# Optimization experiments

Measured on AMD Instinct MI355X. Metric: run time of the kernel, lower is better.

The kernel has to match this reference:

```python
import jax, jax.numpy as jnp
import numpy as np
import math

E, H, KH, F = 2048, 32, 8, 8192
HD = E // H          # 64
KV = KH * HD         # 512
B, S = 2, 2048
EPS = 1e-5


def _rope_table(seq_len, head_dim, base=10000.0):
    inv = 1.0 / (base ** (np.arange(0, head_dim, 2, dtype=np.float32) / head_dim))
    t = np.arange(seq_len, dtype=np.float32)
    fr = np.outer(t, inv)                               # [S, HD/2]
    return jnp.asarray(np.stack([np.cos(fr), np.sin(fr)], axis=-1))  # [S, HD/2, 2]


def setup_inputs() -> dict:
    key = jax.random.key(0)
    ks = jax.random.split(key, 8)
    x = jax.random.normal(ks[0], (B, S, E), dtype=jnp.float32)
    attention_mask = jnp.tril(jnp.ones((1, 1, S, S), dtype=bool))  # causal
    freqs_cis = _rope_table(S, HD)                                  # [S, 32, 2]
    sc = 0.02
    w_qkv = jax.random.normal(ks[1], (E + 2 * KV, E), dtype=jnp.float32) * sc
    w_o = jax.random.normal(ks[2], (E, E), dtype=jnp.float32) * sc
    w1 = jax.random.normal(ks[3], (F, E), dtype=jnp.float32) * sc
    w3 = jax.random.normal(ks[4], (F, E), dtype=jnp.float32) * sc
    w2 = jax.random.normal(ks[5], (E, F), dtype=jnp.float32) * sc
    attn_norm_w = jnp.ones((E,), dtype=jnp.float32)
    ff_norm_w = jnp.ones((E,), dtype=jnp.float32)
    return {"x": x, "attention_mask": attention_mask, "freqs_cis": freqs_cis,
            "w_qkv": w_qkv, "w_o": w_o, "w1": w1, "w2": w2, "w3": w3,
            "attn_norm_w": attn_norm_w, "ff_norm_w": ff_norm_w}


def _rmsnorm(x, w):
    xf = x.astype(jnp.float32)
    n = xf * jax.lax.rsqrt(jnp.mean(xf * xf, axis=-1, keepdims=True) + EPS)
    return n.astype(x.dtype) * w


def _apply_rope(x, freqs_cis):
    # x: [B, h, S, HD]; freqs_cis: [S, HD/2, 2] broadcasting over B, h
    xf = x.astype(jnp.float32).reshape(*x.shape[:-1], -1, 2)
    c, s = freqs_cis[..., 0], freqs_cis[..., 1]
    x0, x1 = xf[..., 0], xf[..., 1]
    out = jnp.stack([x0 * c - x1 * s, x1 * c + x0 * s], axis=-1)
    return out.reshape(x.shape).astype(x.dtype)


def reference(x, attention_mask, freqs_cis, w_qkv, w_o, w1, w2, w3, attn_norm_w, ff_norm_w):
    bs, seq = x.shape[:2]
    h = _rmsnorm(x, attn_norm_w)
    qkv = h @ w_qkv.T                                   # [B, S, E + 2*KV]
    q, k, v = jnp.split(qkv, [E, E + KV], axis=-1)
    q = q.reshape(bs, seq, H, HD).transpose(0, 2, 1, 3)   # [B, H, S, HD]
    k = k.reshape(bs, seq, KH, HD).transpose(0, 2, 1, 3)  # [B, KH, S, HD]
    v = v.reshape(bs, seq, KH, HD).transpose(0, 2, 1, 3)
    q = _apply_rope(q, freqs_cis)
    k = _apply_rope(k, freqs_cis)
    rep = H // KH
    k = jnp.repeat(k, rep, axis=1)                        # [B, H, S, HD]
    v = jnp.repeat(v, rep, axis=1)
    score = jnp.einsum('bhqd,bhkd->bhqk', q, k) / math.sqrt(HD)
    score = jnp.where(attention_mask, score, -jnp.inf)
    attn = jax.nn.softmax(score, axis=-1)
    o = jnp.einsum('bhqk,bhkd->bhqd', attn, v)
    o = o.transpose(0, 2, 1, 3).reshape(bs, seq, E) @ w_o.T
    h2 = x + o
    g = _rmsnorm(h2, ff_norm_w)
    ff = (jax.nn.silu(g @ w1.T) * (g @ w3.T)) @ w2.T
    return h2 + ff
```

## Files before the change

kernel.cpp:

```cpp
#include <hip/hip_runtime.h>
#include <hip/hip_bf16.h>
#include <cstdint>
#include <cstddef>

typedef __bf16 bf16;
typedef __bf16 bf16x2 __attribute__((ext_vector_type(2)));
typedef __bf16 bf16x4 __attribute__((ext_vector_type(4)));
typedef __bf16 bf16x8 __attribute__((ext_vector_type(8)));
typedef float f32x4 __attribute__((ext_vector_type(4)));
typedef float f32x16 __attribute__((ext_vector_type(16)));

#define EDIM 2048
#define SEQ  2048
#define BATCH 2
#define NH   32
#define NKV  8
#define HD   64
#define FF   8192
#define NTOK 4096
#define QKVN 3072

__device__ __forceinline__ void gld_lds16(const void* gp, void* lp) {
    __builtin_amdgcn_global_load_lds(
        (__attribute__((address_space(1))) void*)(gp),
        (__attribute__((address_space(3))) void*)(lp), 16, 0, 0);
}

__global__ __launch_bounds__(256)
void cvt_f32_bf16(const float* __restrict__ in, bf16* __restrict__ out, long n4) {
    long i = (long)blockIdx.x * blockDim.x + threadIdx.x;
    long stride = (long)gridDim.x * blockDim.x;
    for (; i < n4; i += stride) {
        float4 v = ((const float4*)in)[i];
        bf16x4 o;
        o[0] = (bf16)v.x; o[1] = (bf16)v.y; o[2] = (bf16)v.z; o[3] = (bf16)v.w;
        ((bf16x4*)out)[i] = o;
    }
}

__global__ __launch_bounds__(256)
void rmsnorm_bf16(const float* __restrict__ x, const float* __restrict__ w,
                  bf16* __restrict__ out) {
    __shared__ float red[4];
    const int row = blockIdx.x;
    const long base = (long)row * EDIM;
    const int t = threadIdx.x;
    float4 v0 = *(const float4*)(x + base + t * 4);
    float4 v1 = *(const float4*)(x + base + 1024 + t * 4);
    float ss = v0.x*v0.x + v0.y*v0.y + v0.z*v0.z + v0.w*v0.w
             + v1.x*v1.x + v1.y*v1.y + v1.z*v1.z + v1.w*v1.w;
    #pragma unroll
    for (int off = 1; off < 64; off <<= 1) ss += __shfl_xor(ss, off, 64);
    if ((t & 63) == 0) red[t >> 6] = ss;
    __syncthreads();
    float tot = red[0] + red[1] + red[2] + red[3];
    float inv = rsqrtf(tot * (1.0f / EDIM) + 1e-5f);
    float4 w0 = *(const float4*)(w + t * 4);
    float4 w1 = *(const float4*)(w + 1024 + t * 4);
    bf16x4 o0, o1;
    o0[0] = (bf16)(v0.x * inv * w0.x); o0[1] = (bf16)(v0.y * inv * w0.y);
    o0[2] = (bf16)(v0.z * inv * w0.z); o0[3] = (bf16)(v0.w * inv * w0.w);
    o1[0] = (bf16)(v1.x * inv * w1.x); o1[1] = (bf16)(v1.y * inv * w1.y);
    o1[2] = (bf16)(v1.z * inv * w1.z); o1[3] = (bf16)(v1.w * inv * w1.w);
    *(bf16x4*)(out + base + t * 4) = o0;
    *(bf16x4*)(out + base + 1024 + t * 4) = o1;
}

template<int EPI>
__global__ __launch_bounds__(256, 2)
void gemm_nt(const bf16* __restrict__ A, const bf16* __restrict__ B,
             void* __restrict__ Cv, const float* __restrict__ res,
             int M, int N, int K) {
    __shared__ bf16 As[128 * 32];
    __shared__ bf16 Bs[128 * 32];
    const int tid = threadIdx.x;
    const int lane = tid & 63;
    const int wave = tid >> 6;
    const int wm = (wave >> 1) * 64;
    const int wn = (wave & 1) * 64;

    int gx = gridDim.x, gy = gridDim.y;
    int bx = blockIdx.x, by = blockIdx.y;
    int nwg = gx * gy;
    if (((nwg & 63) | (gx & 7) | (gy & 7)) == 0) {
        int l = bx + gx * by;
        int nl = (l & 7) * (nwg >> 3) + (l >> 3);
        int s = nl >> 6, r = nl & 63;
        int spr = gx >> 3;
        bx = (s % spr) * 8 + (r & 7);
        by = (s / spr) * 8 + (r >> 3);
    }
    const int bm = by * 128;
    const int bn = bx * 128;
    const int lrow = lane & 15;
    const int koff = (lane >> 4) * 8;

    f32x4 acc[4][4] = {};

    for (int k0 = 0; k0 < K; k0 += 32) {
        __syncthreads();
        #pragma unroll
        for (int t = 0; t < 2; ++t) {
            int c = tid + t * 256;
            int r = c >> 2;
            int kc = (c & 3) * 8;
            gld_lds16(A + (long)(bm + r) * K + k0 + kc, As + c * 8);
            gld_lds16(B + (long)(bn + r) * K + k0 + kc, Bs + c * 8);
        }
        __syncthreads();
        bf16x8 af[4], bfr[4];
        #pragma unroll
        for (int t = 0; t < 4; ++t) {
            af[t]  = *(const bf16x8*)(As + (wm + t * 16 + lrow) * 32 + koff);
            bfr[t] = *(const bf16x8*)(Bs + (wn + t * 16 + lrow) * 32 + koff);
        }
        #pragma unroll
        for (int i = 0; i < 4; ++i)
            #pragma unroll
            for (int j = 0; j < 4; ++j)
                acc[i][j] = __builtin_amdgcn_mfma_f32_16x16x32_bf16(af[i], bfr[j], acc[i][j], 0, 0, 0);
    }

    const int row0 = bm + wm + (lane >> 4) * 4;
    const int col0 = bn + wn + (lane & 15);
    #pragma unroll
    for (int i = 0; i < 4; ++i) {
        #pragma unroll
        for (int j = 0; j < 4; ++j) {
            int col = col0 + j * 16;
            #pragma unroll
            for (int r = 0; r < 4; ++r) {
                long idx = (long)(row0 + i * 16 + r) * N + col;
                float v = acc[i][j][r];
                if (EPI == 0) {
                    ((float*)Cv)[idx] = v;
                } else if (EPI == 1) {
                    ((bf16*)Cv)[idx] = (bf16)v;
                } else if (EPI == 2) {
                    ((float*)Cv)[idx] = v + res[idx];
                } else {
                    float u = (float)((bf16*)Cv)[idx];
                    float sl = u / (1.0f + __expf(-u));
                    ((bf16*)Cv)[idx] = (bf16)(sl * v);
                }
            }
        }
    }
}

__global__ __launch_bounds__(256)
void rope_prep(const bf16* __restrict__ qkv, const float* __restrict__ fr,
               bf16* __restrict__ Qo, bf16* __restrict__ Ko) {
    const int row = blockIdx.x;
    const int b = row >> 11, s = row & 2047;
    const int t = threadIdx.x;
    const long rbase = (long)row * QKVN;
    #pragma unroll
    for (int i = 0; i < 4; ++i) {
        int p = t + i * 256;
        int hh = p >> 5, d = p & 31;
        bf16x2 xv = *(const bf16x2*)(qkv + rbase + hh * 64 + 2 * d);
        float x0 = (float)xv[0], x1 = (float)xv[1];
        float2 cs = *(const float2*)(fr + (long)(s * 32 + d) * 2);
        bf16x2 o;
        o[0] = (bf16)((x0 * cs.x - x1 * cs.y) * 0.125f);
        o[1] = (bf16)((x1 * cs.x + x0 * cs.y) * 0.125f);
        *(bf16x2*)(Qo + ((long)(b * NH + hh) * SEQ + s) * HD + 2 * d) = o;
    }
    {
        int kh = t >> 5, d = t & 31;
        bf16x2 xv = *(const bf16x2*)(qkv + rbase + EDIM + kh * 64 + 2 * d);
        float x0 = (float)xv[0], x1 = (float)xv[1];
        float2 cs = *(const float2*)(fr + (long)(s * 32 + d) * 2);
        bf16x2 o;
        o[0] = (bf16)(x0 * cs.x - x1 * cs.y);
        o[1] = (bf16)(x1 * cs.x + x0 * cs.y);
        *(bf16x2*)(Ko + ((long)(b * NKV + kh) * SEQ + s) * HD + 2 * d) = o;
    }
}

__global__ __launch_bounds__(256)
void v_prep(const bf16* __restrict__ qkv, bf16* __restrict__ Vt) {
    __shared__ bf16 tile[64 * 72];
    const int blk = blockIdx.x;
    const int b = blk >> 8;
    const int kvh = (blk >> 5) & 7;
    const int st = blk & 31;
    const int t = threadIdx.x;
    #pragma unroll
    for (int i = 0; i < 2; ++i) {
        int c = t + i * 256;
        int kk = c >> 3, hdo = (c & 7) * 8;
        bf16x8 v = *(const bf16x8*)(qkv + (long)(b * SEQ + st * 64 + kk) * QKVN + 2560 + kvh * 64 + hdo);
        *(bf16x8*)(tile + kk * 72 + hdo) = v;
    }
    __syncthreads();
    const long obase = ((long)(b * NKV + kvh) * 32 + st) * 4096;
    #pragma unroll
    for (int i = 0; i < 2; ++i) {
        int c = t + i * 256;
        int hd = c >> 3, ko = (c & 7) * 8;
        bf16x8 v;
        #pragma unroll
        for (int j = 0; j < 8; ++j) v[j] = tile[(ko + j) * 72 + hd];
        *(bf16x8*)(Vt + obase + hd * 64 + ko) = v;
    }
}

__global__ __launch_bounds__(256, 3)
void attn_fwd(const bf16* __restrict__ Q, const bf16* __restrict__ K,
              const bf16* __restrict__ Vt, bf16* __restrict__ Out) {
    __shared__ bf16 Ps[4][32][40];
    const int tid = threadIdx.x, lane = tid & 63, w = tid >> 6;
    const int bh = blockIdx.x;
    const int qt = blockIdx.y;
    const int b = bh >> 5, h = bh & 31;
    const int kvh = h >> 2;
    const int ql = lane & 31;
    const int hh = lane >> 5;
    const int sw = (ql ^ (ql >> 3)) & 3;
    const int q0 = qt * 128 + w * 32;
    const int qmax = q0 + 31;
    const long qbase  = ((long)(b * NH + h) * SEQ + q0) * HD;
    const long kvbase = ((long)(b * NKV + kvh) * SEQ) * HD;
    bf16* Pw = &Ps[w][0][0];

    bf16x8 qa[4];
    #pragma unroll
    for (int ds = 0; ds < 4; ++ds)
        qa[ds] = *(const bf16x8*)(Q + qbase + (long)ql * HD + ds * 16 + hh * 8);

    f32x16 oacc[2] = {};
    float mi = -1e30f, li = 0.f;

    const int nt64 = qt * 2 + 1 + (w >> 1);
    for (int kt = 0; kt < nt64; ++kt) {
        const bf16* Kt  = K  + kvbase + (long)kt * (64 * HD);
        const bf16* Vtt = Vt + kvbase + (long)kt * 4096;
        bf16x8 ka[2][4], va[2][2][2];
        #pragma unroll
        for (int h2 = 0; h2 < 2; ++h2)
            #pragma unroll
            for (int ds = 0; ds < 4; ++ds)
                ka[h2][ds] = *(const bf16x8*)(Kt + (h2 * 32 + ql) * HD + ds * 16 + hh * 8);
        #pragma unroll
        for (int h2 = 0; h2 < 2; ++h2)
            #pragma unroll
            for (int t = 0; t < 2; ++t)
                #pragma unroll
                for (int c = 0; c < 2; ++c)
                    va[h2][t][c] = *(const bf16x8*)(Vtt + (t * 32 + ql) * 64 + h2 * 32 + c * 16 + hh * 8);
        const bool lastt = (kt == nt64 - 1);
        #pragma unroll
        for (int h2 = 0; h2 < 2; ++h2) {
            if (h2 == 1 && kt * 64 + 32 > qmax) break;
            f32x16 s = {};
            #pragma unroll
            for (int ds = 0; ds < 4; ++ds)
                s = __builtin_amdgcn_mfma_f32_32x32x16_bf16(ka[h2][ds], qa[ds], s, 0, 0, 0);
            if (lastt) {
                #pragma unroll
                for (int r = 0; r < 16; ++r) {
                    int kk = kt * 64 + h2 * 32 + (r & 3) + 8 * (r >> 2) + 4 * hh;
                    if (kk > q0 + ql) s[r] = -1e30f;
                }
            }
            float tmax = s[0];
            #pragma unroll
            for (int r = 1; r < 16; ++r) tmax = fmaxf(tmax, s[r]);
            tmax = fmaxf(tmax, __shfl_xor(tmax, 32, 64));
            if (!__all(tmax <= mi)) {
                float mnew = fmaxf(mi, tmax);
                float alpha = __expf(mi - mnew);
                li *= alpha;
                #pragma unroll
                for (int r = 0; r < 16; ++r) { oacc[0][r] *= alpha; oacc[1][r] *= alpha; }
                mi = mnew;
            }
            float psum = 0.f;
            #pragma unroll
            for (int g2 = 0; g2 < 4; ++g2) {
                bf16x4 pw;
                #pragma unroll
                for (int j = 0; j < 4; ++j) {
                    float p = __expf(s[g2 * 4 + j] - mi);
                    psum += p;
                    pw[j] = (bf16)p;
                }
                *(bf16x4*)(Pw + ql * 40 + ((g2 ^ sw) << 3) + 4 * hh) = pw;
            }
            psum += __shfl_xor(psum, 32, 64);
            li += psum;
            bf16x8 p0 = *(const bf16x8*)(Pw + ql * 40 + ((hh ^ sw) << 3));
            bf16x8 p1 = *(const bf16x8*)(Pw + ql * 40 + (((2 + hh) ^ sw) << 3));
            #pragma unroll
            for (int t = 0; t < 2; ++t) {
                oacc[t] = __builtin_amdgcn_mfma_f32_32x32x16_bf16(va[h2][t][0], p0, oacc[t], 0, 0, 0);
                oacc[t] = __builtin_amdgcn_mfma_f32_32x32x16_bf16(va[h2][t][1], p1, oacc[t], 0, 0, 0);
            }
        }
    }

    float inv = 1.0f / li;
    const long obase = ((long)b * SEQ + q0 + ql) * EDIM + h * 64;
    #pragma unroll
    for (int t = 0; t < 2; ++t)
        #pragma unroll
        for (int rg = 0; rg < 4; ++rg) {
            bf16x4 o4;
            #pragma unroll
            for (int j = 0; j < 4; ++j) o4[j] = (bf16)(oacc[t][rg * 4 + j] * inv);
            *(bf16x4*)(Out + obase + t * 32 + rg * 8 + hh * 4) = o4;
        }
}

extern "C" void kernel_launch(void* const* d_in, const int* in_sizes, int n_in,
                              void* d_out, int out_size, void* d_ws, size_t ws_size,
                              hipStream_t stream) {
    const float* x    = (const float*)d_in[0];
    const float* fr   = (const float*)d_in[2];
    const float* wqkv = (const float*)d_in[3];
    const float* wo   = (const float*)d_in[4];
    const float* w1   = (const float*)d_in[5];
    const float* w2   = (const float*)d_in[6];
    const float* w3   = (const float*)d_in[7];
    const float* anw  = (const float*)d_in[8];
    const float* fnw  = (const float*)d_in[9];
    float* out = (float*)d_out;

    const size_t SZ_WQKV = (size_t)QKVN * EDIM;
    const size_t SZ_WO   = (size_t)EDIM * EDIM;
    const size_t SZ_WFF  = (size_t)FF * EDIM;
    const size_t B_WQKV  = SZ_WQKV * 2;
    const size_t B_WO    = SZ_WO * 2;
    const size_t B_WFF   = SZ_WFF * 2;
    const size_t B_HATTN = (size_t)NTOK * EDIM * 2;
    const size_t B_QKV   = (size_t)NTOK * QKVN * 2;
    const size_t B_SCR   = (size_t)NTOK * EDIM * 4;
    const size_t B_FF1   = (size_t)NTOK * FF * 2;
    const size_t NEED = B_WQKV + B_WO + 3 * B_WFF + B_HATTN + B_QKV + B_SCR + B_FF1;
    if (ws_size < NEED) return;

    char* ws = (char*)d_ws;
    size_t off = 0;
    auto alloc = [&](size_t bytes) -> void* {
        void* p = ws + off;
        off += (bytes + 255) & ~(size_t)255;
        return p;
    };
    bf16* wqkv_b = (bf16*)alloc(B_WQKV);
    bf16* wo_b   = (bf16*)alloc(B_WO);
    bf16* w1_b   = (bf16*)alloc(B_WFF);
    bf16* w3_b   = (bf16*)alloc(B_WFF);
    bf16* w2_b   = (bf16*)alloc(B_WFF);
    bf16* h_attn = (bf16*)alloc(B_HATTN);
    bf16* qkv_g  = (bf16*)alloc(B_QKV);
    char* scr    = (char*)alloc(B_SCR);
    bf16* Qb  = (bf16*)scr;
    bf16* Kb  = (bf16*)(scr + (size_t)BATCH * NH * SEQ * HD * 2);
    bf16* Vtb = (bf16*)(scr + (size_t)BATCH * (NH + NKV) * SEQ * HD * 2);
    float* h2 = (float*)scr;
    bf16* ff1 = (bf16*)alloc(B_FF1);
    bf16* g_b = qkv_g;

    cvt_f32_bf16<<<512, 256, 0, stream>>>(wqkv, wqkv_b, (long)(SZ_WQKV / 4));
    cvt_f32_bf16<<<512, 256, 0, stream>>>(wo,   wo_b,   (long)(SZ_WO / 4));
    cvt_f32_bf16<<<512, 256, 0, stream>>>(w1,   w1_b,   (long)(SZ_WFF / 4));
    cvt_f32_bf16<<<512, 256, 0, stream>>>(w3,   w3_b,   (long)(SZ_WFF / 4));
    cvt_f32_bf16<<<512, 256, 0, stream>>>(w2,   w2_b,   (long)(SZ_WFF / 4));
    rmsnorm_bf16<<<NTOK, 256, 0, stream>>>(x, anw, h_attn);
    gemm_nt<1><<<dim3(QKVN / 128, NTOK / 128), 256, 0, stream>>>(
        h_attn, wqkv_b, qkv_g, nullptr, NTOK, QKVN, EDIM);
    rope_prep<<<NTOK, 256, 0, stream>>>(qkv_g, fr, Qb, Kb);
    v_prep<<<BATCH * NKV * (SEQ / 64), 256, 0, stream>>>(qkv_g, Vtb);
    attn_fwd<<<dim3(BATCH * NH, SEQ / 128), 256, 0, stream>>>(Qb, Kb, Vtb, h_attn);
    gemm_nt<2><<<dim3(EDIM / 128, NTOK / 128), 256, 0, stream>>>(
        h_attn, wo_b, h2, x, NTOK, EDIM, EDIM);
    rmsnorm_bf16<<<NTOK, 256, 0, stream>>>(h2, fnw, g_b);
    gemm_nt<1><<<dim3(FF / 128, NTOK / 128), 256, 0, stream>>>(
        g_b, w1_b, ff1, nullptr, NTOK, FF, EDIM);
    gemm_nt<3><<<dim3(FF / 128, NTOK / 128), 256, 0, stream>>>(
        g_b, w3_b, ff1, nullptr, NTOK, FF, EDIM);
    gemm_nt<2><<<dim3(EDIM / 128, NTOK / 128), 256, 0, stream>>>(
        ff1, w2_b, out, h2, NTOK, EDIM, FF);
    (void)in_sizes; (void)n_in; (void)out_size; (void)ws_size;
}
```

Before: 1.114 ms.

## Add 256x256 multi-buffered GEMM kernel for QKV and FFN up-projections

Introduces a new 512-thread GEMM with 256x256 tiles and a 4-slot LDS ring buffer (128KB dynamic shared memory). Loads are issued three stages ahead with explicit vmcnt waits and barriers so global-to-LDS copies overlap MFMA work. The new kernel replaces the 128x128 GEMM for the QKV, w1 and w3 projections to get more reuse per tile and better latency hiding. The old GEMM's launch bound is raised to 4 blocks per CU, and its XCD remap is factored into a helper. The large tile gives fewer blocks (e.g. 192 for QKV), which risks poor CU occupancy, and the explicit wait counts must be exactly right.

```diff
diff --git a/kernel.cpp b/kernel.cpp
--- a/kernel.cpp
+++ b/kernel.cpp
@@ -24,6 +24,19 @@
     __builtin_amdgcn_global_load_lds(
         (__attribute__((address_space(1))) void*)(gp),
         (__attribute__((address_space(3))) void*)(lp), 16, 0, 0);
+}
+
+__device__ __forceinline__ void remap_xcd(int& bx, int& by) {
+    int gx = gridDim.x, gy = gridDim.y;
+    int nwg = gx * gy;
+    if (((nwg & 63) | (gx & 7) | (gy & 7)) == 0) {
+        int l = bx + gx * by;
+        int nl = (l & 7) * (nwg >> 3) + (l >> 3);
+        int s = nl >> 6, r = nl & 63;
+        int spr = gx >> 3;
+        bx = (s % spr) * 8 + (r & 7);
+        by = (s / spr) * 8 + (r >> 3);
+    }
 }
 
 __global__ __launch_bounds__(256)
@@ -67,7 +80,7 @@
 }
 
 template<int EPI>
-__global__ __launch_bounds__(256, 2)
+__global__ __launch_bounds__(256, 4)
 void gemm_nt(const bf16* __restrict__ A, const bf16* __restrict__ B,
              void* __restrict__ Cv, const float* __restrict__ res,
              int M, int N, int K) {
@@ -79,17 +92,8 @@
     const int wm = (wave >> 1) * 64;
     const int wn = (wave & 1) * 64;
 
-    int gx = gridDim.x, gy = gridDim.y;
     int bx = blockIdx.x, by = blockIdx.y;
-    int nwg = gx * gy;
-    if (((nwg & 63) | (gx & 7) | (gy & 7)) == 0) {
-        int l = bx + gx * by;
-        int nl = (l & 7) * (nwg >> 3) + (l >> 3);
-        int s = nl >> 6, r = nl & 63;
-        int spr = gx >> 3;
-        bx = (s % spr) * 8 + (r & 7);
-        by = (s / spr) * 8 + (r >> 3);
-    }
+    remap_xcd(bx, by);
     const int bm = by * 128;
     const int bn = bx * 128;
     const int lrow = lane & 15;
@@ -136,8 +140,110 @@
                     ((float*)Cv)[idx] = v;
                 } else if (EPI == 1) {
                     ((bf16*)Cv)[idx] = (bf16)v;
-                } else if (EPI == 2) {
+                } else {
                     ((float*)Cv)[idx] = v + res[idx];
+                }
+            }
+        }
+    }
+}
+
+#define G2_BUFE 16384
+
+template<int VN, bool STG>
+__device__ __forceinline__ void g2_phase(
+    bf16* __restrict__ smem, int buf,
+    const bf16* __restrict__ pa, const bf16* __restrict__ pb,
+    long kstage, long rstep, int tid,
+    const int (&aoff)[8], const int (&boff)[4], f32x4 (&acc)[8][4])
+{
+    const bf16* base = smem + buf * G2_BUFE;
+    bf16x8 af[8], bfr[4];
+    #pragma unroll
+    for (int i = 0; i < 8; ++i) af[i] = *(const bf16x8*)(base + aoff[i]);
+    #pragma unroll
+    for (int j = 0; j < 4; ++j) bfr[j] = *(const bf16x8*)(base + boff[j]);
+    if (STG) {
+        bf16* d = smem + ((buf + 3) & 3) * G2_BUFE + tid * 8;
+        gld_lds16(pa + kstage,         d);
+        gld_lds16(pa + kstage + rstep, d + 4096);
+        gld_lds16(pb + kstage,         d + 8192);
+        gld_lds16(pb + kstage + rstep, d + 8192 + 4096);
+    }
+    asm volatile("s_waitcnt vmcnt(%0)" :: "n"(VN) : "memory");
+    __builtin_amdgcn_s_barrier();
+    __builtin_amdgcn_sched_barrier(0);
+    asm volatile("s_waitcnt lgkmcnt(0)" ::: "memory");
+    __builtin_amdgcn_sched_barrier(0);
+    __builtin_amdgcn_s_setprio(1);
+    #pragma unroll
+    for (int i = 0; i < 8; ++i)
+        #pragma unroll
+        for (int j = 0; j < 4; ++j)
+            acc[i][j] = __builtin_amdgcn_mfma_f32_16x16x32_bf16(af[i], bfr[j], acc[i][j], 0, 0, 0);
+    __builtin_amdgcn_s_setprio(0);
+    __builtin_amdgcn_s_barrier();
+    __builtin_amdgcn_sched_barrier(0);
+}
+
+template<int EPI>
+__global__ __launch_bounds__(512, 2)
+void gemm256_nt(const bf16* __restrict__ A, const bf16* __restrict__ B,
+                void* __restrict__ Cv, const float* __restrict__ res,
+                int M, int N, int K) {
+    extern __shared__ bf16 smem[];
+    const int tid = threadIdx.x;
+    const int lane = tid & 63, wave = tid >> 6;
+    const int wr = wave >> 2, wc = wave & 3;
+    const int lrow = lane & 15, g = lane >> 4;
+    int bx = blockIdx.x, by = blockIdx.y;
+    remap_xcd(bx, by);
+    const int bm = by * 256, bn = bx * 256;
+    const long Kl = (long)K;
+    const bf16* pa = A + (long)(bm + (tid >> 2)) * Kl + (tid & 3) * 8;
+    const bf16* pb = B + (long)(bn + (tid >> 2)) * Kl + (tid & 3) * 8;
+    const long rstep = 128 * Kl;
+    int aoff[8], boff[4];
+    #pragma unroll
+    for (int i = 0; i < 8; ++i) aoff[i] = (wr * 128 + i * 16 + lrow) * 32 + g * 8;
+    #pragma unroll
+    for (int j = 0; j < 4; ++j) boff[j] = 8192 + (wc * 64 + j * 16 + lrow) * 32 + g * 8;
+
+    f32x4 acc[8][4] = {};
+
+    #pragma unroll
+    for (int t = 0; t < 3; ++t) {
+        bf16* d = smem + t * G2_BUFE + tid * 8;
+        gld_lds16(pa + t * 32,         d);
+        gld_lds16(pa + t * 32 + rstep, d + 4096);
+        gld_lds16(pb + t * 32,         d + 8192);
+        gld_lds16(pb + t * 32 + rstep, d + 8192 + 4096);
+    }
+    asm volatile("s_waitcnt vmcnt(8)" ::: "memory");
+    __builtin_amdgcn_s_barrier();
+    __builtin_amdgcn_sched_barrier(0);
+
+    const int NT = K >> 5;
+    int t = 0;
+    for (; t < NT - 3; ++t)
+        g2_phase<8, true >(smem, t & 3, pa, pb, (long)(t + 3) * 32, rstep, tid, aoff, boff, acc);
+    g2_phase<4, false>(smem, t & 3, pa, pb, 0, rstep, tid, aoff, boff, acc); ++t;
+    g2_phase<0, false>(smem, t & 3, pa, pb, 0, rstep, tid, aoff, boff, acc); ++t;
+    g2_phase<0, false>(smem, t & 3, pa, pb, 0, rstep, tid, aoff, boff, acc);
+
+    const int row0 = bm + wr * 128 + g * 4;
+    const int col0 = bn + wc * 64 + lrow;
+    #pragma unroll
+    for (int i = 0; i < 8; ++i) {
+        #pragma unroll
+        for (int j = 0; j < 4; ++j) {
+            int col = col0 + j * 16;
+            #pragma unroll
+            for (int r = 0; r < 4; ++r) {
+                long idx = (long)(row0 + i * 16 + r) * N + col;
+                float v = acc[i][j][r];
+                if (EPI == 1) {
+                    ((bf16*)Cv)[idx] = (bf16)v;
                 } else {
                     float u = (float)((bf16*)Cv)[idx];
                     float sl = u / (1.0f + __expf(-u));
@@ -146,6 +252,7 @@
             }
         }
     }
+    (void)res;
 }
 
 __global__ __launch_bounds__(256)
@@ -327,6 +434,15 @@
     const float* anw  = (const float*)d_in[8];
     const float* fnw  = (const float*)d_in[9];
     float* out = (float*)d_out;
+
+    static int attr_done = 0;
+    if (!attr_done) {
+        hipFuncSetAttribute(reinterpret_cast<const void*>(gemm256_nt<1>),
+                            hipFuncAttributeMaxDynamicSharedMemorySize, 131072);
+        hipFuncSetAttribute(reinterpret_cast<const void*>(gemm256_nt<3>),
+                            hipFuncAttributeMaxDynamicSharedMemorySize, 131072);
+        attr_done = 1;
+    }
 
     const size_t SZ_WQKV = (size_t)QKVN * EDIM;
     const size_t SZ_WO   = (size_t)EDIM * EDIM;
@@ -369,7 +485,7 @@
     cvt_f32_bf16<<<512, 256, 0, stream>>>(w3,   w3_b,   (long)(SZ_WFF / 4));
     cvt_f32_bf16<<<512, 256, 0, stream>>>(w2,   w2_b,   (long)(SZ_WFF / 4));
     rmsnorm_bf16<<<NTOK, 256, 0, stream>>>(x, anw, h_attn);
-    gemm_nt<1><<<dim3(QKVN / 128, NTOK / 128), 256, 0, stream>>>(
+    gemm256_nt<1><<<dim3(QKVN / 256, NTOK / 256), 512, 131072, stream>>>(
         h_attn, wqkv_b, qkv_g, nullptr, NTOK, QKVN, EDIM);
     rope_prep<<<NTOK, 256, 0, stream>>>(qkv_g, fr, Qb, Kb);
     v_prep<<<BATCH * NKV * (SEQ / 64), 256, 0, stream>>>(qkv_g, Vtb);
@@ -377,9 +493,9 @@
     gemm_nt<2><<<dim3(EDIM / 128, NTOK / 128), 256, 0, stream>>>(
         h_attn, wo_b, h2, x, NTOK, EDIM, EDIM);
     rmsnorm_bf16<<<NTOK, 256, 0, stream>>>(h2, fnw, g_b);
-    gemm_nt<1><<<dim3(FF / 128, NTOK / 128), 256, 0, stream>>>(
+    gemm256_nt<1><<<dim3(FF / 256, NTOK / 256), 512, 131072, stream>>>(
         g_b, w1_b, ff1, nullptr, NTOK, FF, EDIM);
-    gemm_nt<3><<<dim3(FF / 128, NTOK / 128), 256, 0, stream>>>(
+    gemm256_nt<3><<<dim3(FF / 256, NTOK / 256), 512, 131072, stream>>>(
         g_b, w3_b, ff1, nullptr, NTOK, FF, EDIM);
     gemm_nt<2><<<dim3(EDIM / 128, NTOK / 128), 256, 0, stream>>>(
         ff1, w2_b, out, h2, NTOK, EDIM, FF);
```

Result: no change. 1.102 ms (-1.1%).
